# Kernel optimization log

Hardware: AMD Instinct MI355X
Metric: run time of the kernel (lower is better)

The kernel has to match this reference:

```python
import jax, jax.numpy as jnp
import numpy as np

DIM = 1536
N_HEADS = 12
HEAD_DIM = DIM // N_HEADS          # 128
C = HEAD_DIM // 2                  # 64 complex channels
C_F = C - 2 * (C // 3)             # 22
C_H = C // 3                       # 21
C_W = C // 3                       # 21
EPS = 1e-6
MAX_F, MAX_HW = 64, 64


def _rope_table(max_len, c_sub):
    # Wan rope_params: theta_j = 10000^{-j/c_sub}, angle = pos * theta
    inv = 1.0 / (10000.0 ** (np.arange(c_sub, dtype=np.float32) / c_sub))
    ang = np.arange(max_len, dtype=np.float32)[:, None] * inv[None, :]
    return jnp.asarray(np.cos(ang)), jnp.asarray(np.sin(ang))


def setup_inputs() -> dict:
    key = jax.random.key(0)
    ks = jax.random.split(key, 12)
    s = 1.0 / np.sqrt(DIM)
    F_, H_, W_ = 9, 16, 28
    S = F_ * H_ * W_
    x = jax.random.normal(ks[0], (1, S, DIM), dtype=jnp.float32)
    Wq = jax.random.normal(ks[1], (DIM, DIM), dtype=jnp.float32) * s
    Wk = jax.random.normal(ks[2], (DIM, DIM), dtype=jnp.float32) * s
    Wv = jax.random.normal(ks[3], (DIM, DIM), dtype=jnp.float32) * s
    Wo = jax.random.normal(ks[4], (DIM, DIM), dtype=jnp.float32) * s
    bq = jnp.zeros((DIM,), jnp.float32)
    bk = jnp.zeros((DIM,), jnp.float32)
    bv = jnp.zeros((DIM,), jnp.float32)
    bo = jnp.zeros((DIM,), jnp.float32)
    gq = jnp.ones((DIM,), jnp.float32)
    gk = jnp.ones((DIM,), jnp.float32)
    cos_f, sin_f = _rope_table(MAX_F, C_F)
    cos_h, sin_h = _rope_table(MAX_HW, C_H)
    cos_w, sin_w = _rope_table(MAX_HW, C_W)
    return dict(x=x, Wq=Wq, bq=bq, Wk=Wk, bk=bk, Wv=Wv, bv=bv, Wo=Wo, bo=bo,
                gq=gq, gk=gk, cos_f=cos_f, sin_f=sin_f, cos_h=cos_h,
                sin_h=sin_h, cos_w=cos_w, sin_w=sin_w, F=F_, H=H_, W=W_)


def _rms(t, g):
    t = t.astype(jnp.float32)
    return t * jax.lax.rsqrt(jnp.mean(t * t, axis=-1, keepdims=True) + EPS) * g


def _grid_cos_sin(cos_f, sin_f, cos_h, sin_h, cos_w, sin_w, F, H, W):
    # concat per-axis angle tables expanded over the (F,H,W) grid -> [S, C]
    def expand(tab, shape):
        return jnp.broadcast_to(tab.reshape(shape + (tab.shape[-1],)), (F, H, W, tab.shape[-1]))
    cos = jnp.concatenate([expand(cos_f[:F], (F, 1, 1)),
                           expand(cos_h[:H], (1, H, 1)),
                           expand(cos_w[:W], (1, 1, W))], axis=-1).reshape(F * H * W, C)
    sin = jnp.concatenate([expand(sin_f[:F], (F, 1, 1)),
                           expand(sin_h[:H], (1, H, 1)),
                           expand(sin_w[:W], (1, 1, W))], axis=-1).reshape(F * H * W, C)
    return cos, sin


def _rope(t, cos, sin):
    # t: [B,S,N,D]; adjacent pairs (even=real, odd=imag) rotated by complex freqs
    b, s, n, d = t.shape
    tr = t.reshape(b, s, n, C, 2)
    e, o = tr[..., 0], tr[..., 1]
    co = cos[None, :, None, :]
    si = sin[None, :, None, :]
    return jnp.stack([e * co - o * si, e * si + o * co], axis=-1).reshape(b, s, n, d)


def reference(x, Wq, bq, Wk, bk, Wv, bv, Wo, bo, gq, gk,
              cos_f, sin_f, cos_h, sin_h, cos_w, sin_w, F, H, W):
    b, s, dim = x.shape
    q = _rms(x @ Wq.T + bq, gq).reshape(b, s, N_HEADS, HEAD_DIM)
    k = _rms(x @ Wk.T + bk, gk).reshape(b, s, N_HEADS, HEAD_DIM)
    v = (x @ Wv.T + bv).reshape(b, s, N_HEADS, HEAD_DIM)
    cos, sin = _grid_cos_sin(cos_f, sin_f, cos_h, sin_h, cos_w, sin_w, F, H, W)
    rq = _rope(q, cos, sin)
    rk = _rope(k, cos, sin)
    scale = 1.0 / jnp.sqrt(jnp.asarray(HEAD_DIM, jnp.float32))
    scores = jnp.einsum('bqhd,bkhd->bhqk', rq, rk) * scale
    att = jax.nn.softmax(scores, axis=-1)
    out = jnp.einsum('bhqk,bkhd->bqhd', att, v).reshape(b, s, dim)
    return out @ Wo.T + bo
```

## Files before the change

kernel.cpp:

```cpp
#include <hip/hip_runtime.h>
#include <math.h>

using u16 = unsigned short;
using u32 = unsigned int;

typedef __attribute__((ext_vector_type(8))) short short8;
typedef __attribute__((ext_vector_type(4))) float float4v;

#define S_LEN 4032
#define DIM   1536
#define NH    12
#define HD    128
#define F_DIM 9
#define H_DIM 16
#define W_DIM 28
#define NX4 1548288
#define NW4 589824

__device__ __forceinline__ float b2f(u16 v) {
  return __uint_as_float(((u32)v) << 16);
}
__device__ __forceinline__ u16 f2bf(float f) {
  u32 u = __float_as_uint(f);
  u32 r = (u + 0x7FFFu + ((u >> 16) & 1u)) >> 16;
  return (u16)r;
}
__device__ __forceinline__ u32 pack2(float lo, float hi) {
  return __builtin_amdgcn_perm(__float_as_uint(hi), __float_as_uint(lo),
                               0x07060302u);
}

__device__ __forceinline__ void gld16(const void* g, void* l) {
  __builtin_amdgcn_global_load_lds(
      (const __attribute__((address_space(1))) void*)g,
      (__attribute__((address_space(3))) void*)l, 16, 0, 0);
}

__device__ __forceinline__ void plswap(u32 a, u32 b, u32& x, u32& y, int lane) {
#if __has_builtin(__builtin_amdgcn_permlane32_swap) && __has_builtin(__builtin_amdgcn_permlane16_swap)
  auto t = __builtin_amdgcn_permlane32_swap(a, b, false, false);
  auto u = __builtin_amdgcn_permlane16_swap(t[0], t[1], false, false);
  x = u[0]; y = u[1];
#else
  u32 ax = (u32)__shfl_xor((int)a, 32, 64), bx = (u32)__shfl_xor((int)b, 32, 64);
  u32 t0 = (lane & 32) ? bx : a;
  u32 t1 = (lane & 32) ? b : ax;
  u32 t0x = (u32)__shfl_xor((int)t0, 16, 64), t1x = (u32)__shfl_xor((int)t1, 16, 64);
  x = (lane & 16) ? t1x : t0;
  y = (lane & 16) ? t1 : t0x;
#endif
}

__global__ void __launch_bounds__(256) cast_all(
    const float* __restrict__ x, const float* __restrict__ wq,
    const float* __restrict__ wk, const float* __restrict__ wv,
    const float* __restrict__ wo,
    u16* __restrict__ xb, u16* __restrict__ wqb,
    u16* __restrict__ wkb, u16* __restrict__ wvb,
    u16* __restrict__ wob)
{
  int i = blockIdx.x * 256 + threadIdx.x;
  const float* s; u16* d; int j;
  if (i < NX4)              { s = x;  d = xb;  j = i; }
  else if (i < NX4 + NW4)   { s = wq; d = wqb; j = i - NX4; }
  else if (i < NX4 + 2*NW4) { s = wk; d = wkb; j = i - NX4 - NW4; }
  else if (i < NX4 + 3*NW4) { s = wv; d = wvb; j = i - NX4 - 2*NW4; }
  else                      { s = wo; d = wob; j = i - NX4 - 3*NW4; }
  const float4 v = ((const float4*)s)[j];
  ushort4 o;
  o.x = f2bf(v.x); o.y = f2bf(v.y); o.z = f2bf(v.z); o.w = f2bf(v.w);
  ((ushort4*)d)[j] = o;
}

__global__ void __launch_bounds__(256) gemm_qkv_fused(
    const u16* __restrict__ X,
    const u16* __restrict__ Wq, const u16* __restrict__ Wk, const u16* __restrict__ Wv,
    const float* __restrict__ bq, const float* __restrict__ bk, const float* __restrict__ bv,
    u16* __restrict__ Qb, u16* __restrict__ Kb, u16* __restrict__ Vb)
{
  __shared__ u16 As[2][128 * 64];
  __shared__ u16 Bs[2][3][64 * 64];
  const int tid  = threadIdx.x;
  const int wave = tid >> 6, lane = tid & 63;
  const int quad = lane >> 4, l15 = lane & 15;
  const int wm = wave >> 1, wn = wave & 1;
  const int bm = blockIdx.y * 128, bn = blockIdx.x * 64;

  float4v acc[3][4][2] = {};

  const int arow = lane >> 3;
  const int acol = ((lane & 7) ^ arow) * 8;

  auto stage = [&](int b, int kt) {
#pragma unroll
    for (int c = 0; c < 4; ++c) {
      int seg = wave * 4 + c;
      int row = seg * 8 + arow;
      int ga = bm + row; if (ga > S_LEN - 1) ga = S_LEN - 1;
      gld16(&X[(size_t)ga * DIM + kt + acol], &As[b][seg * 512]);
    }
#pragma unroll
    for (int z = 0; z < 3; ++z) {
      const u16* W = (z == 0) ? Wq : (z == 1) ? Wk : Wv;
#pragma unroll
      for (int c = 0; c < 2; ++c) {
        int seg = wave * 2 + c;
        int row = seg * 8 + arow;
        gld16(&W[(size_t)(bn + row) * DIM + kt + acol], &Bs[b][z][seg * 512]);
      }
    }
  };

  stage(0, 0);
  __syncthreads();

  int cur = 0;
  for (int kt = 0; kt < DIM; kt += 64) {
    if (kt + 64 < DIM) stage(cur ^ 1, kt + 64);

#pragma unroll
    for (int ks = 0; ks < 64; ks += 32) {
      const int kc = ks >> 3;
      short8 af[4];
#pragma unroll
      for (int mt = 0; mt < 4; ++mt) {
        const int ra = wm * 64 + mt * 16 + l15;
        af[mt] = *(const short8*)((const char*)As[cur] + ra * 128 + (((kc + quad) ^ (ra & 7)) << 4));
      }
#pragma unroll
      for (int z = 0; z < 3; ++z) {
        short8 bf[2];
#pragma unroll
        for (int nt = 0; nt < 2; ++nt) {
          const int rb = wn * 32 + nt * 16 + l15;
          bf[nt] = *(const short8*)((const char*)Bs[cur][z] + rb * 128 + (((kc + quad) ^ (rb & 7)) << 4));
        }
#pragma unroll
        for (int mt = 0; mt < 4; ++mt)
#pragma unroll
          for (int nt = 0; nt < 2; ++nt)
            acc[z][mt][nt] = __builtin_amdgcn_mfma_f32_16x16x32_bf16(af[mt], bf[nt], acc[z][mt][nt], 0, 0, 0);
      }
    }

    __syncthreads();
    cur ^= 1;
  }

#pragma unroll
  for (int z = 0; z < 3; ++z) {
    u16* O          = (z == 0) ? Qb : (z == 1) ? Kb : Vb;
    const float* bi = (z == 0) ? bq : (z == 1) ? bk : bv;
#pragma unroll
    for (int mt = 0; mt < 4; ++mt) {
      const int row = bm + wm * 64 + mt * 16 + quad * 4;
#pragma unroll
      for (int nt = 0; nt < 2; ++nt) {
        const int col = bn + wn * 32 + nt * 16 + l15;
        const float bv_ = bi[col];
#pragma unroll
        for (int r = 0; r < 4; ++r) {
          float v = acc[z][mt][nt][r] + bv_;
          if (row + r < S_LEN)
            O[(size_t)(row + r) * DIM + col] = f2bf(v);
        }
      }
    }
  }
}

template <bool F32OUT>
__device__ __forceinline__ void gemm_core(
    const u16* __restrict__ A, const u16* __restrict__ Bw,
    const float* __restrict__ bias, void* __restrict__ OutV,
    int bm, int bn)
{
  __shared__ u16 As[2][128 * 64];
  __shared__ u16 Bs[2][128 * 64];
  const int tid  = threadIdx.x;
  const int wave = tid >> 6, lane = tid & 63;
  const int quad = lane >> 4, l15 = lane & 15;
  const int wm = wave >> 1, wn = wave & 1;

  float4v acc[4][4] = {};

  const int arow = lane >> 3;
  const int acol = ((lane & 7) ^ arow) * 8;

  auto stage = [&](int b, int kt) {
#pragma unroll
    for (int c = 0; c < 4; ++c) {
      int seg = wave * 4 + c;
      int row = seg * 8 + arow;
      int ga = bm + row; if (ga > S_LEN - 1) ga = S_LEN - 1;
      gld16(&A[(size_t)ga * DIM + kt + acol], &As[b][seg * 512]);
      gld16(&Bw[(size_t)(bn + row) * DIM + kt + acol], &Bs[b][seg * 512]);
    }
  };

  stage(0, 0);
  __syncthreads();

  int cur = 0;
  for (int kt = 0; kt < DIM; kt += 64) {
    if (kt + 64 < DIM) stage(cur ^ 1, kt + 64);

#pragma unroll
    for (int ks = 0; ks < 64; ks += 32) {
      const int kc = ks >> 3;
      short8 af[4], bf[4];
#pragma unroll
      for (int mt = 0; mt < 4; ++mt) {
        const int ra = wm * 64 + mt * 16 + l15;
        af[mt] = *(const short8*)((const char*)As[cur] + ra * 128 + (((kc + quad) ^ (ra & 7)) << 4));
      }
#pragma unroll
      for (int nt = 0; nt < 4; ++nt) {
        const int rb = wn * 64 + nt * 16 + l15;
        bf[nt] = *(const short8*)((const char*)Bs[cur] + rb * 128 + (((kc + quad) ^ (rb & 7)) << 4));
      }
#pragma unroll
      for (int mt = 0; mt < 4; ++mt)
#pragma unroll
        for (int nt = 0; nt < 4; ++nt)
          acc[mt][nt] = __builtin_amdgcn_mfma_f32_16x16x32_bf16(af[mt], bf[nt], acc[mt][nt], 0, 0, 0);
    }

    __syncthreads();
    cur ^= 1;
  }

#pragma unroll
  for (int mt = 0; mt < 4; ++mt) {
    const int row = bm + wm * 64 + mt * 16 + quad * 4;
#pragma unroll
    for (int nt = 0; nt < 4; ++nt) {
      const int col = bn + wn * 64 + nt * 16 + l15;
      const float bv = bias[col];
#pragma unroll
      for (int r = 0; r < 4; ++r) {
        float v = acc[mt][nt][r] + bv;
        if (row + r < S_LEN) {
          if (F32OUT) ((float*)OutV)[(size_t)(row + r) * DIM + col] = v;
          else        ((u16*)OutV)[(size_t)(row + r) * DIM + col] = f2bf(v);
        }
      }
    }
  }
}

__global__ void __launch_bounds__(256) gemm_wo(
    const u16* __restrict__ A, const u16* __restrict__ Wo,
    const float* __restrict__ bo, float* __restrict__ Out)
{
  gemm_core<true>(A, Wo, bo, Out, blockIdx.y * 128, blockIdx.x * 128);
}

__global__ void __launch_bounds__(256) rms_rope(
    u16* Q, u16* K,
    const float* __restrict__ gq, const float* __restrict__ gk,
    const float* __restrict__ cf, const float* __restrict__ sf,
    const float* __restrict__ ch, const float* __restrict__ sh,
    const float* __restrict__ cw, const float* __restrict__ sw)
{
  __shared__ float red[2][4];
  const int s = blockIdx.x;
  const int t = threadIdx.x;
  const int wave = t >> 6, lane = t & 63;
  const size_t rowb = (size_t)s * DIM + t * 6;

  u32* q32 = (u32*)(Q + rowb);
  u32* k32 = (u32*)(K + rowb);
  u32 qw[3], kw[3];
#pragma unroll
  for (int j = 0; j < 3; ++j) { qw[j] = q32[j]; kw[j] = k32[j]; }

  float sq = 0.f, sk = 0.f;
#pragma unroll
  for (int j = 0; j < 3; ++j) {
    float a0 = b2f((u16)qw[j]), a1 = b2f((u16)(qw[j] >> 16));
    float b0 = b2f((u16)kw[j]), b1 = b2f((u16)(kw[j] >> 16));
    sq += a0 * a0 + a1 * a1;
    sk += b0 * b0 + b1 * b1;
  }
#pragma unroll
  for (int m = 1; m < 64; m <<= 1) {
    sq += __shfl_xor(sq, m, 64);
    sk += __shfl_xor(sk, m, 64);
  }
  if (lane == 0) { red[0][wave] = sq; red[1][wave] = sk; }
  __syncthreads();
  const float tq = red[0][0] + red[0][1] + red[0][2] + red[0][3];
  const float tk = red[1][0] + red[1][1] + red[1][2] + red[1][3];
  const float scq = rsqrtf(tq * (1.0f / DIM) + 1e-6f);
  const float sck = rsqrtf(tk * (1.0f / DIM) + 1e-6f);

  const int f  = s / (H_DIM * W_DIM);
  const int hh = (s / W_DIM) % H_DIM;
  const int w  = s % W_DIM;

#pragma unroll
  for (int j = 0; j < 3; ++j) {
    const int pi = t * 3 + j;
    const int c = pi & 63;
    float co, si;
    if (c < 22)      { co = cf[f * 22 + c];        si = sf[f * 22 + c]; }
    else if (c < 43) { co = ch[hh * 21 + c - 22];  si = sh[hh * 21 + c - 22]; }
    else             { co = cw[w * 21 + c - 43];   si = sw[w * 21 + c - 43]; }
    const int gi = 2 * pi;
    const float2 gqv = *(const float2*)&gq[gi];
    const float2 gkv = *(const float2*)&gk[gi];
    {
      float e = b2f((u16)qw[j])         * scq * gqv.x;
      float o = b2f((u16)(qw[j] >> 16)) * scq * gqv.y;
      q32[j] = (u32)f2bf(e * co - o * si) | ((u32)f2bf(e * si + o * co) << 16);
    }
    {
      float e = b2f((u16)kw[j])         * sck * gkv.x;
      float o = b2f((u16)(kw[j] >> 16)) * sck * gkv.y;
      k32[j] = (u32)f2bf(e * co - o * si) | ((u32)f2bf(e * si + o * co) << 16);
    }
  }
}

__global__ void __launch_bounds__(256) transpose_v(
    const u16* __restrict__ V, u16* __restrict__ Vt)
{
  __shared__ u16 tile[64][65];
  const int s0 = blockIdx.x * 64, d0 = blockIdx.y * 64;
  const int t = threadIdx.x;
#pragma unroll
  for (int i = 0; i < 16; ++i) {
    int idx = t + i * 256; int rr = idx >> 6, cc = idx & 63;
    tile[rr][cc] = V[(size_t)(s0 + rr) * DIM + d0 + cc];
  }
  __syncthreads();
#pragma unroll
  for (int i = 0; i < 16; ++i) {
    int idx = t + i * 256; int rr = idx >> 6, cc = idx & 63;
    Vt[(size_t)(d0 + rr) * S_LEN + s0 + cc] = tile[cc][rr];
  }
}

__global__ void __launch_bounds__(256, 2) attn_kernel(
    const u16* __restrict__ rq, const u16* __restrict__ rk,
    const u16* __restrict__ vt,
    u16* __restrict__ po, float* __restrict__ pl, int klen)
{
  __shared__ u16 Ks[64 * 128];
  __shared__ u16 Vs[128 * 64];

  const int id    = blockIdx.x;
  const int xcd   = id & 7;
  const int rest  = id >> 3;
  const int band  = rest / 21;
  const int slot  = rest - band * 21;
  const int slice = band * 8 + xcd;
  const int h     = slice % NH;
  const int split = slice / NH;
  const int k_begin = split * klen;
  const int k_end   = (k_begin + klen < S_LEN) ? (k_begin + klen) : S_LEN;
  const int qb = slot * 192;
  const int tid = threadIdx.x, wave = tid >> 6, lane = tid & 63;
  const int quad = lane >> 4, l15 = lane & 15;
  const int q0 = qb + wave * 48;

  const int kr_l   = (lane >> 4);
  const int kc_l   = lane & 15;
  const int vdr_l  = (lane >> 3);
  const int vc_l   = lane & 7;

  short8 qf[3][4];
#pragma unroll
  for (int mt = 0; mt < 3; ++mt) {
    int row = q0 + mt * 16 + l15; if (row > S_LEN - 1) row = S_LEN - 1;
#pragma unroll
    for (int c = 0; c < 4; ++c)
      qf[mt][c] = *(const short8*)&rq[(size_t)row * DIM + h * HD + c * 32 + quad * 8];
  }

  float4v o[3][8] = {};
  float l_[3] = {0.f, 0.f, 0.f};

  const float SC = 0.08838834764831845f * 1.4426950408889634f;
  const float M0 = 20.0f;

#pragma unroll
  for (int c = 0; c < 4; ++c) {
    const int seg = wave * 4 + c;
    const int kr = seg * 4 + kr_l;
    gld16(&rk[(size_t)(k_begin + kr) * DIM + h * HD + ((kc_l ^ (kr & 15)) << 3)],
          &Ks[seg * 512]);
  }
  __syncthreads();

  for (int kt = k_begin; kt < k_end; kt += 64) {
#pragma unroll
    for (int c = 0; c < 4; ++c) {
      const int seg = wave * 4 + c;
      const int vd = seg * 8 + vdr_l;
      gld16(&vt[(size_t)(h * HD + vd) * S_LEN + kt + ((vc_l ^ (vd & 7)) << 3)],
            &Vs[seg * 512]);
    }

    short8 pf[3][2];

#pragma unroll
    for (int half = 0; half < 2; ++half) {
      float4v sc[3][2] = {};
      __builtin_amdgcn_s_setprio(1);
#pragma unroll
      for (int nth = 0; nth < 2; ++nth) {
        const int krow = (half * 2 + nth) * 16 + l15;
#pragma unroll
        for (int c = 0; c < 4; ++c) {
          const short8 kf = *(const short8*)((char*)Ks + krow * 256 + (((c * 4 + quad) ^ l15) << 4));
#pragma unroll
          for (int mt = 0; mt < 3; ++mt)
            sc[mt][nth] = __builtin_amdgcn_mfma_f32_16x16x32_bf16(kf, qf[mt][c], sc[mt][nth], 0, 0, 0);
        }
      }
      __builtin_amdgcn_s_setprio(0);

#pragma unroll
      for (int mt = 0; mt < 3; ++mt) {
        u32 W[2][2];
#pragma unroll
        for (int nth = 0; nth < 2; ++nth) {
          const float p0 = __builtin_amdgcn_exp2f(fmaf(sc[mt][nth][0], SC, -M0));
          const float p1 = __builtin_amdgcn_exp2f(fmaf(sc[mt][nth][1], SC, -M0));
          const float p2 = __builtin_amdgcn_exp2f(fmaf(sc[mt][nth][2], SC, -M0));
          const float p3 = __builtin_amdgcn_exp2f(fmaf(sc[mt][nth][3], SC, -M0));
          l_[mt] += (p0 + p1) + (p2 + p3);
          W[nth][0] = pack2(p0, p1);
          W[nth][1] = pack2(p2, p3);
        }
        u32 w0, w1, w2, w3;
        plswap(W[0][0], W[1][0], w0, w2, lane);
        plswap(W[0][1], W[1][1], w1, w3, lane);
        union { u32 w[4]; short8 s; } cv;
        cv.w[0] = w0; cv.w[1] = w1; cv.w[2] = w2; cv.w[3] = w3;
        pf[mt][half] = cv.s;
      }
    }

    __syncthreads();

    if (kt + 64 < k_end) {
#pragma unroll
      for (int c = 0; c < 4; ++c) {
        const int seg = wave * 4 + c;
        const int kr = seg * 4 + kr_l;
        gld16(&rk[(size_t)(kt + 64 + kr) * DIM + h * HD + ((kc_l ^ (kr & 15)) << 3)],
              &Ks[seg * 512]);
      }
    }

    __builtin_amdgcn_s_setprio(1);
#pragma unroll
    for (int dt = 0; dt < 8; ++dt) {
      const int drow = dt * 16 + l15;
#pragma unroll
      for (int ko = 0; ko < 2; ++ko) {
        const short8 vf = *(const short8*)((char*)Vs + drow * 128 + (((ko * 4 + quad) ^ (l15 & 7)) << 4));
#pragma unroll
        for (int mt = 0; mt < 3; ++mt)
          o[mt][dt] = __builtin_amdgcn_mfma_f32_16x16x32_bf16(vf, pf[mt][ko], o[mt][dt], 0, 0, 0);
      }
    }
    __builtin_amdgcn_s_setprio(0);

    __syncthreads();
  }

#pragma unroll
  for (int mt = 0; mt < 3; ++mt) {
    float t = l_[mt];
    t += __shfl_xor(t, 16, 64);
    t += __shfl_xor(t, 32, 64);
    l_[mt] = t;
  }
#pragma unroll
  for (int mt = 0; mt < 3; ++mt) {
    const int q = q0 + mt * 16 + l15;
    const bool valid = q < S_LEN;
    const size_t rbase = ((size_t)(split * NH + h) * S_LEN + q) * HD;
#pragma unroll
    for (int dt = 0; dt < 8; ++dt) {
      if (valid) {
        ushort4 pk;
        pk.x = f2bf(o[mt][dt][0]); pk.y = f2bf(o[mt][dt][1]);
        pk.z = f2bf(o[mt][dt][2]); pk.w = f2bf(o[mt][dt][3]);
        *(ushort4*)&po[rbase + dt * 16 + quad * 4] = pk;
      }
    }
    if (quad == 0 && valid)
      pl[(size_t)(split * NH + h) * S_LEN + q] = l_[mt];
  }
}

__global__ void __launch_bounds__(256) attn_merge(
    const u16* __restrict__ po, const float* __restrict__ pl,
    u16* __restrict__ ao, int nsplit)
{
  const int gw = (blockIdx.x * 256 + threadIdx.x) >> 6;
  const int lane = threadIdx.x & 63;
  const int h = gw / S_LEN;
  const int q = gw - h * S_LEN;
  float den = 0.f, a0 = 0.f, a1 = 0.f;
  for (int s = 0; s < nsplit; ++s) {
    const size_t r = (size_t)(s * NH + h) * S_LEN + q;
    den += pl[r];
    const ushort2 v = *(const ushort2*)&po[r * HD + lane * 2];
    a0 += b2f(v.x); a1 += b2f(v.y);
  }
  const float inv = (den > 0.f) ? (1.0f / den) : 0.f;
  ushort2 out;
  out.x = f2bf(a0 * inv);
  out.y = f2bf(a1 * inv);
  *(ushort2*)&ao[(size_t)q * DIM + h * HD + lane * 2] = out;
}

extern "C" void kernel_launch(void* const* d_in, const int* in_sizes, int n_in,
                              void* d_out, int out_size, void* d_ws, size_t ws_size,
                              hipStream_t stream) {
  const float* x  = (const float*)d_in[0];
  const float* Wq = (const float*)d_in[1];
  const float* bq = (const float*)d_in[2];
  const float* Wk = (const float*)d_in[3];
  const float* bk = (const float*)d_in[4];
  const float* Wv = (const float*)d_in[5];
  const float* bv = (const float*)d_in[6];
  const float* Wo = (const float*)d_in[7];
  const float* bo = (const float*)d_in[8];
  const float* gq = (const float*)d_in[9];
  const float* gk = (const float*)d_in[10];
  const float* cf = (const float*)d_in[11];
  const float* sf = (const float*)d_in[12];
  const float* ch = (const float*)d_in[13];
  const float* sh = (const float*)d_in[14];
  const float* cw = (const float*)d_in[15];
  const float* sw = (const float*)d_in[16];

  char* ws = (char*)d_ws;
  const size_t sz  = (size_t)S_LEN * DIM * 2;
  const size_t wsz = (size_t)DIM * DIM * 2;
  u16* Xb  = (u16*)(ws);
  u16* Qb  = (u16*)(ws + sz);
  u16* Kb  = (u16*)(ws + 2 * sz);
  u16* Vb  = (u16*)(ws + 3 * sz);
  u16* Wqb = (u16*)(ws + 4 * sz);
  u16* Wkb = (u16*)(ws + 4 * sz + wsz);
  u16* Wvb = (u16*)(ws + 4 * sz + 2 * wsz);

  const int nsplit = 2;
  const int klen   = 2048;
  const size_t po_one = (size_t)NH * S_LEN * HD * 2;
  const size_t pl_one = (size_t)NH * S_LEN * 4;
  char* pbase = ws + 4 * sz;
  u16*   po = (u16*)pbase;
  float* pl = (float*)(pbase + (size_t)nsplit * po_one);
  u16* Wob = (u16*)(ws + 4 * sz + (size_t)nsplit * (po_one + pl_one));
  u16* Vt  = Xb;
  u16* Ao  = Qb;

  cast_all<<<(NX4 + 4 * NW4) / 256, 256, 0, stream>>>(
      x, Wq, Wk, Wv, Wo, Xb, Wqb, Wkb, Wvb, Wob);

  gemm_qkv_fused<<<dim3(24, 32), 256, 0, stream>>>(
      Xb, Wqb, Wkb, Wvb, bq, bk, bv, Qb, Kb, Vb);

  rms_rope<<<S_LEN, 256, 0, stream>>>(Qb, Kb, gq, gk, cf, sf, ch, sh, cw, sw);
  transpose_v<<<dim3(63, 24), 256, 0, stream>>>(Vb, Vt);
  attn_kernel<<<504, 256, 0, stream>>>(Qb, Kb, Vt, po, pl, klen);
  attn_merge<<<(NH * S_LEN) / 4, 256, 0, stream>>>(po, pl, Ao, nsplit);
  gemm_wo<<<dim3(12, 32), 256, 0, stream>>>(Ao, Wob, bo, (float*)d_out);
}
```

Measured before the change: 382.4 us.

## Double-buffer K and V tiles in LDS for attention kernel

Makes the K and V shared-memory tiles two buffers each and prefetches the next K/V tile into the alternate buffer at the start of every iteration. This drops the mid-iteration barrier and the late K reload, so global-to-LDS copies overlap with both the QK and PV MFMA phases. It doubles the LDS footprint per block, which may limit how many blocks fit per CU.

After: 381.0 us, median of 2. About the same (-0.4%).

```diff
diff --git a/kernel.cpp b/kernel.cpp
--- a/kernel.cpp
+++ b/kernel.cpp
@@ -347,8 +347,8 @@
     const u16* __restrict__ vt,
     u16* __restrict__ po, float* __restrict__ pl, int klen)
 {
-  __shared__ u16 Ks[64 * 128];
-  __shared__ u16 Vs[128 * 64];
+  __shared__ u16 Ks[2][64 * 128];
+  __shared__ u16 Vs[2][128 * 64];
 
   const int id    = blockIdx.x;
   const int xcd   = id & 7;
@@ -370,38 +370,52 @@
   const int vdr_l  = (lane >> 3);
   const int vc_l   = lane & 7;
 
-  short8 qf[3][4];
-#pragma unroll
-  for (int mt = 0; mt < 3; ++mt) {
-    int row = q0 + mt * 16 + l15; if (row > S_LEN - 1) row = S_LEN - 1;
-#pragma unroll
-    for (int c = 0; c < 4; ++c)
-      qf[mt][c] = *(const short8*)&rq[(size_t)row * DIM + h * HD + c * 32 + quad * 8];
-  }
-
-  float4v o[3][8] = {};
-  float l_[3] = {0.f, 0.f, 0.f};
-
-  const float SC = 0.08838834764831845f * 1.4426950408889634f;
-  const float M0 = 20.0f;
-
-#pragma unroll
-  for (int c = 0; c < 4; ++c) {
-    const int seg = wave * 4 + c;
-    const int kr = seg * 4 + kr_l;
-    gld16(&rk[(size_t)(k_begin + kr) * DIM + h * HD + ((kc_l ^ (kr & 15)) << 3)],
-          &Ks[seg * 512]);
-  }
-  __syncthreads();
-
-  for (int kt = k_begin; kt < k_end; kt += 64) {
+  auto stageK = [&](int b, int kt) {
+#pragma unroll
+    for (int c = 0; c < 4; ++c) {
+      const int seg = wave * 4 + c;
+      const int kr = seg * 4 + kr_l;
+      gld16(&rk[(size_t)(kt + kr) * DIM + h * HD + ((kc_l ^ (kr & 15)) << 3)],
+            &Ks[b][seg * 512]);
+    }
+  };
+  auto stageV = [&](int b, int kt) {
 #pragma unroll
     for (int c = 0; c < 4; ++c) {
       const int seg = wave * 4 + c;
       const int vd = seg * 8 + vdr_l;
       gld16(&vt[(size_t)(h * HD + vd) * S_LEN + kt + ((vc_l ^ (vd & 7)) << 3)],
-            &Vs[seg * 512]);
-    }
+            &Vs[b][seg * 512]);
+    }
+  };
+
+  short8 qf[3][4];
+#pragma unroll
+  for (int mt = 0; mt < 3; ++mt) {
+    int row = q0 + mt * 16 + l15; if (row > S_LEN - 1) row = S_LEN - 1;
+#pragma unroll
+    for (int c = 0; c < 4; ++c)
+      qf[mt][c] = *(const short8*)&rq[(size_t)row * DIM + h * HD + c * 32 + quad * 8];
+  }
+
+  float4v o[3][8] = {};
+  float l_[3] = {0.f, 0.f, 0.f};
+
+  const float SC = 0.08838834764831845f * 1.4426950408889634f;
+  const float M0 = 20.0f;
+
+  stageK(0, k_begin);
+  stageV(0, k_begin);
+  __syncthreads();
+
+  int cur = 0;
+  for (int kt = k_begin; kt < k_end; kt += 64) {
+    if (kt + 64 < k_end) {
+      stageK(cur ^ 1, kt + 64);
+      stageV(cur ^ 1, kt + 64);
+    }
+    const char* KsC = (const char*)Ks[cur];
+    const char* VsC = (const char*)Vs[cur];
 
     short8 pf[3][2];
 
@@ -414,7 +428,7 @@
         const int krow = (half * 2 + nth) * 16 + l15;
 #pragma unroll
         for (int c = 0; c < 4; ++c) {
-          const short8 kf = *(const short8*)((char*)Ks + krow * 256 + (((c * 4 + quad) ^ l15) << 4));
+          const short8 kf = *(const short8*)(KsC + krow * 256 + (((c * 4 + quad) ^ l15) << 4));
 #pragma unroll
           for (int mt = 0; mt < 3; ++mt)
             sc[mt][nth] = __builtin_amdgcn_mfma_f32_16x16x32_bf16(kf, qf[mt][c], sc[mt][nth], 0, 0, 0);
@@ -444,25 +458,13 @@
       }
     }
 
-    __syncthreads();
-
-    if (kt + 64 < k_end) {
-#pragma unroll
-      for (int c = 0; c < 4; ++c) {
-        const int seg = wave * 4 + c;
-        const int kr = seg * 4 + kr_l;
-        gld16(&rk[(size_t)(kt + 64 + kr) * DIM + h * HD + ((kc_l ^ (kr & 15)) << 3)],
-              &Ks[seg * 512]);
-      }
-    }
-
     __builtin_amdgcn_s_setprio(1);
 #pragma unroll
     for (int dt = 0; dt < 8; ++dt) {
       const int drow = dt * 16 + l15;
 #pragma unroll
       for (int ko = 0; ko < 2; ++ko) {
-        const short8 vf = *(const short8*)((char*)Vs + drow * 128 + (((ko * 4 + quad) ^ (l15 & 7)) << 4));
+        const short8 vf = *(const short8*)(VsC + drow * 128 + (((ko * 4 + quad) ^ (l15 & 7)) << 4));
 #pragma unroll
         for (int mt = 0; mt < 3; ++mt)
           o[mt][dt] = __builtin_amdgcn_mfma_f32_16x16x32_bf16(vf, pf[mt][ko], o[mt][dt], 0, 0, 0);
@@ -471,6 +473,7 @@
     __builtin_amdgcn_s_setprio(0);
 
     __syncthreads();
+    cur ^= 1;
   }
 
 #pragma unroll
```
